# Kernel optimization log

Measured on AMD Instinct MI355X. Metric: run time of the kernel, lower is better.

## Reference

```python
import jax, jax.numpy as jnp
import numpy as np

DIM = 64
SQRT_DIM = float(np.sqrt(DIM))


def setup_inputs() -> dict:
    rng = jax.random.key(0)
    k1, k2, k3, k4 = jax.random.split(rng, 4)
    B, S, D = 16, 2048, DIM
    query = jax.random.normal(k1, (B, S, D), dtype=jnp.float32)
    key = jax.random.normal(k2, (B, S, D), dtype=jnp.float32)
    value = jax.random.normal(k3, (B, S, D), dtype=jnp.float32)
    mask = jax.random.randint(k4, (B, S), 0, 2) == 1  # True = masked (pad)
    return {"query": query, "key": key, "value": value, "mask": mask}


def reference(query, key, value, mask):
    # score: [B, S, S]
    score = jnp.einsum('bsd,btd->bst', query, key) / SQRT_DIM
    # symmetric mask: position (i, j) masked if token i OR token j is padded
    m = jnp.logical_or(mask[:, :, None], mask[:, None, :])  # [B, S, S]
    score = jnp.where(m, -jnp.inf, score)
    attn = jax.nn.softmax(score, axis=-1)
    attn = jnp.where(m, 0.0, attn)
    context = jnp.einsum('bst,btd->bsd', attn, value)
    return (context, attn)
```

## Files before the change

### kernel.cpp

```cpp
#include <hip/hip_runtime.h>
#include <hip/hip_bf16.h>

#define NBATCH 16
#define SLEN   2048
#define DIM    64
#define TQ     64
#define NTHR   256
#define NW     4
#define PANEL  128
#define NPANEL (SLEN / PANEL)
#define PROWK  72
#define PROWV  136
#define PROWP  136

typedef __attribute__((ext_vector_type(8))) short bf16x8;
typedef __attribute__((ext_vector_type(4))) float f32x4;

__device__ inline short f2bf(float f) {
    union { __hip_bfloat16 h; short s; } u;
    u.h = __float2bfloat16(f);
    return u.s;
}
__device__ inline float bf2f(unsigned short s) {
    union { unsigned u; float f; } x;
    x.u = ((unsigned)s) << 16;
    return x.f;
}
__device__ inline bf16x8 pack8(float4 a, float4 b) {
    bf16x8 r;
    r[0] = f2bf(a.x); r[1] = f2bf(a.y); r[2] = f2bf(a.z); r[3] = f2bf(a.w);
    r[4] = f2bf(b.x); r[5] = f2bf(b.y); r[6] = f2bf(b.z); r[7] = f2bf(b.w);
    return r;
}

__global__ __launch_bounds__(NTHR, 3) void sdpa_kernel(
    const float* __restrict__ Q, const float* __restrict__ K,
    const float* __restrict__ V, const int* __restrict__ M,
    float* __restrict__ outCtx, float* __restrict__ outAttn)
{
    __shared__ __align__(16) short sK[128 * PROWK];
    __shared__ __align__(16) short sVT[64 * PROWV];
    __shared__ __align__(16) short sP[NW * 16 * PROWP];
    __shared__ float sMask[PANEL];

    const int tid = threadIdx.x;
    const int w = tid >> 6, l = tid & 63, g = l >> 4, c = l & 15;
    const int b  = blockIdx.x >> 5;
    const int i0 = (blockIdx.x & 31) * TQ;
    const int i0w = i0 + w * 16;

    const float* Kb = K + (size_t)b * SLEN * DIM;
    const float* Vb = V + (size_t)b * SLEN * DIM;
    const int*   Mb = M + b * SLEN;

    bf16x8 qa0, qa1;
    {
        const float* qp = Q + ((size_t)b * SLEN + i0w + c) * DIM + g * 8;
        qa0 = pack8(*(const float4*)(qp),      *(const float4*)(qp + 4));
        qa1 = pack8(*(const float4*)(qp + 32), *(const float4*)(qp + 36));
    }

    const float scl = 0.125f;
    float rsum[4] = {0.f, 0.f, 0.f, 0.f};

    for (int p = 0; p < NPANEL; p++) {
        const int j0 = p * PANEL;
        #pragma unroll
        for (int it = 0; it < 8; it++) {
            const int idx = it * NTHR + tid;
            const int row = idx >> 4, c4 = idx & 15;
            float4 kv = *(const float4*)(Kb + (size_t)(j0 + row) * DIM + c4 * 4);
            *(short4*)(sK + row * PROWK + c4 * 4) =
                make_short4(f2bf(kv.x), f2bf(kv.y), f2bf(kv.z), f2bf(kv.w));
        }
        if (tid < PANEL) sMask[tid] = Mb[j0 + tid] ? 0.f : 1.f;
        __syncthreads();
        #pragma unroll
        for (int jt = 0; jt < 8; jt++) {
            const short* kr = sK + (jt * 16 + c) * PROWK + g * 8;
            bf16x8 kb0 = *(const bf16x8*)(kr);
            bf16x8 kb1 = *(const bf16x8*)(kr + 32);
            f32x4 acc = {0.f, 0.f, 0.f, 0.f};
            acc = __builtin_amdgcn_mfma_f32_16x16x32_bf16(qa0, kb0, acc, 0, 0, 0);
            acc = __builtin_amdgcn_mfma_f32_16x16x32_bf16(qa1, kb1, acc, 0, 0, 0);
            const float em = sMask[jt * 16 + c];
            #pragma unroll
            for (int r = 0; r < 4; r++)
                rsum[r] += __expf(acc[r] * scl) * em;
        }
        __syncthreads();
    }
    #pragma unroll
    for (int off = 1; off < 16; off <<= 1) {
        #pragma unroll
        for (int r = 0; r < 4; r++)
            rsum[r] += __shfl_xor(rsum[r], off, 64);
    }
    float scv[4];
    #pragma unroll
    for (int r = 0; r < 4; r++) {
        const int rm = Mb[i0w + g * 4 + r];
        scv[r] = (rm || rsum[r] <= 0.f) ? 0.f : 1.f / rsum[r];
    }

    short* sPw = sP + w * 16 * PROWP;
    f32x4 pv[4];
    #pragma unroll
    for (int nt = 0; nt < 4; nt++) pv[nt] = (f32x4){0.f, 0.f, 0.f, 0.f};

    for (int p = 0; p < NPANEL; p++) {
        const int j0 = p * PANEL;
        #pragma unroll
        for (int it = 0; it < 8; it++) {
            const int idx = it * NTHR + tid;
            const int row = idx >> 4, c4 = idx & 15;
            float4 kv = *(const float4*)(Kb + (size_t)(j0 + row) * DIM + c4 * 4);
            *(short4*)(sK + row * PROWK + c4 * 4) =
                make_short4(f2bf(kv.x), f2bf(kv.y), f2bf(kv.z), f2bf(kv.w));
        }
        #pragma unroll
        for (int it = 0; it < 2; it++) {
            const int task = it * NTHR + tid;
            const int k4 = task >> 4, d4g = task & 15;
            const int kb = k4 * 4, d4 = d4g * 4;
            const int colb = kb ^ ((d4g & 3) << 3);
            const float* vp = Vb + (size_t)(j0 + kb) * DIM + d4;
            float4 r0 = *(const float4*)(vp);
            float4 r1 = *(const float4*)(vp + DIM);
            float4 r2 = *(const float4*)(vp + 2 * DIM);
            float4 r3 = *(const float4*)(vp + 3 * DIM);
            *(short4*)(sVT + (d4 + 0) * PROWV + colb) =
                make_short4(f2bf(r0.x), f2bf(r1.x), f2bf(r2.x), f2bf(r3.x));
            *(short4*)(sVT + (d4 + 1) * PROWV + colb) =
                make_short4(f2bf(r0.y), f2bf(r1.y), f2bf(r2.y), f2bf(r3.y));
            *(short4*)(sVT + (d4 + 2) * PROWV + colb) =
                make_short4(f2bf(r0.z), f2bf(r1.z), f2bf(r2.z), f2bf(r3.z));
            *(short4*)(sVT + (d4 + 3) * PROWV + colb) =
                make_short4(f2bf(r0.w), f2bf(r1.w), f2bf(r2.w), f2bf(r3.w));
        }
        if (tid < PANEL) sMask[tid] = Mb[j0 + tid] ? 0.f : 1.f;
        __syncthreads();

        #pragma unroll
        for (int jt = 0; jt < 8; jt++) {
            const short* kr = sK + (jt * 16 + c) * PROWK + g * 8;
            bf16x8 kb0 = *(const bf16x8*)(kr);
            bf16x8 kb1 = *(const bf16x8*)(kr + 32);
            f32x4 acc = {0.f, 0.f, 0.f, 0.f};
            acc = __builtin_amdgcn_mfma_f32_16x16x32_bf16(qa0, kb0, acc, 0, 0, 0);
            acc = __builtin_amdgcn_mfma_f32_16x16x32_bf16(qa1, kb1, acc, 0, 0, 0);
            const float em = sMask[jt * 16 + c];
            #pragma unroll
            for (int r = 0; r < 4; r++)
                sPw[(g * 4 + r) * PROWP + jt * 16 + c] =
                    f2bf(__expf(acc[r] * scl) * em * scv[r]);
        }

        #pragma unroll
        for (int ks = 0; ks < 4; ks++) {
            bf16x8 af = *(const bf16x8*)(sPw + c * PROWP + ks * 32 + g * 8);
            #pragma unroll
            for (int nt = 0; nt < 4; nt++) {
                const int d = nt * 16 + c;
                const int gp = g ^ ((d >> 2) & 3);
                bf16x8 bfrag = *(const bf16x8*)(sVT + d * PROWV + ks * 32 + gp * 8);
                pv[nt] = __builtin_amdgcn_mfma_f32_16x16x32_bf16(af, bfrag, pv[nt], 0, 0, 0);
            }
        }

        const size_t rowBase = (size_t)b * SLEN + i0w;
        #pragma unroll
        for (int it = 0; it < 8; it++) {
            const int idx = it * 64 + l;
            const int row = idx >> 5, col4 = idx & 31;
            const unsigned short* pp = (const unsigned short*)sPw + row * PROWP + col4 * 4;
            ushort4 p4 = *(const ushort4*)(pp);
            float4 o = {bf2f(p4.x), bf2f(p4.y), bf2f(p4.z), bf2f(p4.w)};
            *(float4*)(outAttn + (rowBase + row) * SLEN + j0 + col4 * 4) = o;
        }
        __syncthreads();
    }

    #pragma unroll
    for (int nt = 0; nt < 4; nt++) {
        #pragma unroll
        for (int r = 0; r < 4; r++)
            outCtx[((size_t)b * SLEN + i0w + g * 4 + r) * DIM + nt * 16 + c] = pv[nt][r];
    }
}

extern "C" void kernel_launch(void* const* d_in, const int* in_sizes, int n_in,
                              void* d_out, int out_size, void* d_ws, size_t ws_size,
                              hipStream_t stream) {
    const float* Q = (const float*)d_in[0];
    const float* K = (const float*)d_in[1];
    const float* V = (const float*)d_in[2];
    const int*   M = (const int*)d_in[3];
    float* outCtx  = (float*)d_out;
    float* outAttn = (float*)d_out + (size_t)NBATCH * SLEN * DIM;
    dim3 grid(NBATCH * (SLEN / TQ));
    sdpa_kernel<<<grid, NTHR, 0, stream>>>(Q, K, V, M, outCtx, outAttn);
}
```

Before: 375.5 us.

## Preconvert K/V to swizzled bf16 workspace and stage panels via direct-to-LDS loads

Adds a pre-pass kernel that converts K to bf16 and V to transposed bf16 in a workspace, both XOR-swizzled, so every attention block no longer re-reads fp32 K/V and converts it for each panel. The main kernel stages panels with global_load_lds, double-buffers K during the row-sum pass, caches the whole mask row in LDS, and folds the 1/sqrt(d) scale into Q. It costs an extra kernel launch and workspace traffic, and lowers the occupancy hint from 3 to 2. A fallback keeps the original kernel when no workspace is available.

```diff
diff --git a/kernel.cpp b/kernel.cpp
--- a/kernel.cpp
+++ b/kernel.cpp
@@ -9,9 +9,9 @@
 #define NW     4
 #define PANEL  128
 #define NPANEL (SLEN / PANEL)
+#define PROWP  136
 #define PROWK  72
 #define PROWV  136
-#define PROWP  136
 
 typedef __attribute__((ext_vector_type(8))) short bf16x8;
 typedef __attribute__((ext_vector_type(4))) float f32x4;
@@ -32,8 +32,208 @@
     r[4] = f2bf(b.x); r[5] = f2bf(b.y); r[6] = f2bf(b.z); r[7] = f2bf(b.w);
     return r;
 }
-
-__global__ __launch_bounds__(NTHR, 3) void sdpa_kernel(
+__device__ inline bf16x8 pack8s(float4 a, float4 b, float s) {
+    bf16x8 r;
+    r[0] = f2bf(a.x * s); r[1] = f2bf(a.y * s); r[2] = f2bf(a.z * s); r[3] = f2bf(a.w * s);
+    r[4] = f2bf(b.x * s); r[5] = f2bf(b.y * s); r[6] = f2bf(b.z * s); r[7] = f2bf(b.w * s);
+    return r;
+}
+
+__global__ __launch_bounds__(256) void preconvert_kernel(
+    const float* __restrict__ K, const float* __restrict__ V,
+    short* __restrict__ Kws, short* __restrict__ VTws)
+{
+    const int b  = blockIdx.x >> 4;
+    const int p  = blockIdx.x & 15;
+    const int j0 = p * PANEL;
+    const int tid = threadIdx.x;
+    const float* Kb = K + ((size_t)b * SLEN + j0) * DIM;
+    const float* Vb = V + ((size_t)b * SLEN + j0) * DIM;
+    short* Kwb  = Kws  + ((size_t)b * SLEN + j0) * DIM;
+    short* VTwb = VTws + (size_t)b * DIM * SLEN;
+
+    #pragma unroll
+    for (int it = 0; it < 8; it++) {
+        const int idx = it * 256 + tid;
+        const int row = idx >> 4, c4 = idx & 15;
+        float4 kv = *(const float4*)(Kb + (size_t)row * DIM + c4 * 4);
+        const int blk = (c4 >> 1) ^ (row & 7);
+        *(short4*)(Kwb + (size_t)row * DIM + blk * 8 + (c4 & 1) * 4) =
+            make_short4(f2bf(kv.x), f2bf(kv.y), f2bf(kv.z), f2bf(kv.w));
+    }
+    #pragma unroll
+    for (int it = 0; it < 2; it++) {
+        const int task = it * 256 + tid;
+        const int k4 = task >> 4, d4 = (task & 15) * 4;
+        const int kb = k4 * 4;
+        const float* vp = Vb + (size_t)kb * DIM + d4;
+        float4 r0 = *(const float4*)(vp);
+        float4 r1 = *(const float4*)(vp + DIM);
+        float4 r2 = *(const float4*)(vp + 2 * DIM);
+        float4 r3 = *(const float4*)(vp + 3 * DIM);
+        const int qn = kb >> 3, hw = kb & 7;
+        *(short4*)(VTwb + (size_t)(d4 + 0) * SLEN + j0 + ((qn ^ ((d4 + 0) & 7)) * 8) + hw) =
+            make_short4(f2bf(r0.x), f2bf(r1.x), f2bf(r2.x), f2bf(r3.x));
+        *(short4*)(VTwb + (size_t)(d4 + 1) * SLEN + j0 + ((qn ^ ((d4 + 1) & 7)) * 8) + hw) =
+            make_short4(f2bf(r0.y), f2bf(r1.y), f2bf(r2.y), f2bf(r3.y));
+        *(short4*)(VTwb + (size_t)(d4 + 2) * SLEN + j0 + ((qn ^ ((d4 + 2) & 7)) * 8) + hw) =
+            make_short4(f2bf(r0.z), f2bf(r1.z), f2bf(r2.z), f2bf(r3.z));
+        *(short4*)(VTwb + (size_t)(d4 + 3) * SLEN + j0 + ((qn ^ ((d4 + 3) & 7)) * 8) + hw) =
+            make_short4(f2bf(r0.w), f2bf(r1.w), f2bf(r2.w), f2bf(r3.w));
+    }
+}
+
+__device__ __forceinline__ void stage_k_panel(const short* __restrict__ Kwb, int j0,
+                                              short* sdst, int w, int l) {
+    const short* src = Kwb + (size_t)j0 * DIM + w * 512 + l * 8;
+    short* dst = sdst + w * 512;
+    #pragma unroll
+    for (int i = 0; i < 4; i++)
+        __builtin_amdgcn_global_load_lds((const unsigned int*)(src + i * 2048),
+                                         (unsigned int*)(dst + i * 2048), 16, 0, 0);
+}
+__device__ __forceinline__ void stage_v_panel(const short* __restrict__ VTwb, int j0,
+                                              short* sdst, int w, int l) {
+    #pragma unroll
+    for (int i = 0; i < 4; i++) {
+        const int d0 = (w * 4 + i) * 4;
+        __builtin_amdgcn_global_load_lds(
+            (const unsigned int*)(VTwb + (size_t)(d0 + (l >> 4)) * SLEN + j0 + (l & 15) * 8),
+            (unsigned int*)(sdst + d0 * PANEL), 16, 0, 0);
+    }
+}
+
+#define MFMA16(a, bb, cc) __builtin_amdgcn_mfma_f32_16x16x32_bf16((a), (bb), (cc), 0, 0, 0)
+
+__global__ __launch_bounds__(NTHR, 2) void sdpa_kernel(
+    const float* __restrict__ Q, const short* __restrict__ Kws,
+    const short* __restrict__ VTws, const int* __restrict__ M,
+    float* __restrict__ outCtx, float* __restrict__ outAttn)
+{
+    __shared__ __align__(16) short sK[PANEL * DIM];
+    __shared__ __align__(16) short sVT[DIM * PANEL];
+    __shared__ __align__(16) short sP[NW * 16 * PROWP];
+    __shared__ float sMaskAll[SLEN];
+
+    const int tid = threadIdx.x;
+    const int w = tid >> 6, l = tid & 63, g = l >> 4, c = l & 15;
+    const int b  = blockIdx.x >> 5;
+    const int i0 = (blockIdx.x & 31) * TQ;
+    const int i0w = i0 + w * 16;
+
+    const short* Kwb  = Kws  + (size_t)b * SLEN * DIM;
+    const short* VTwb = VTws + (size_t)b * DIM * SLEN;
+    const int*   Mb   = M + b * SLEN;
+
+    bf16x8 qa0, qa1;
+    {
+        const float* qp = Q + ((size_t)b * SLEN + i0w + c) * DIM + g * 8;
+        qa0 = pack8s(*(const float4*)(qp),      *(const float4*)(qp + 4),  0.125f);
+        qa1 = pack8s(*(const float4*)(qp + 32), *(const float4*)(qp + 36), 0.125f);
+    }
+
+    #pragma unroll
+    for (int i = 0; i < 8; i++)
+        sMaskAll[i * NTHR + tid] = Mb[i * NTHR + tid] ? 0.f : 1.f;
+    stage_k_panel(Kwb, 0, sK, w, l);
+    __syncthreads();
+
+    float rsum[4] = {0.f, 0.f, 0.f, 0.f};
+    for (int p = 0; p < NPANEL; p++) {
+        const short* cur = (p & 1) ? sVT : sK;
+        if (p < NPANEL - 1)
+            stage_k_panel(Kwb, (p + 1) * PANEL, (p & 1) ? sK : sVT, w, l);
+        const int j0 = p * PANEL;
+        #pragma unroll
+        for (int jt = 0; jt < 8; jt++) {
+            const short* kr = cur + (jt * 16 + c) * DIM;
+            bf16x8 kb0 = *(const bf16x8*)(kr + ((g ^ (c & 7)) * 8));
+            bf16x8 kb1 = *(const bf16x8*)(kr + (((g + 4) ^ (c & 7)) * 8));
+            f32x4 acc = {0.f, 0.f, 0.f, 0.f};
+            acc = MFMA16(qa0, kb0, acc);
+            acc = MFMA16(qa1, kb1, acc);
+            const float em = sMaskAll[j0 + jt * 16 + c];
+            #pragma unroll
+            for (int r = 0; r < 4; r++)
+                rsum[r] += __expf(acc[r]) * em;
+        }
+        __syncthreads();
+    }
+    #pragma unroll
+    for (int off = 1; off < 16; off <<= 1) {
+        #pragma unroll
+        for (int r = 0; r < 4; r++)
+            rsum[r] += __shfl_xor(rsum[r], off, 64);
+    }
+    float scv[4];
+    #pragma unroll
+    for (int r = 0; r < 4; r++) {
+        const float rm = sMaskAll[i0w + g * 4 + r];
+        scv[r] = (rm == 0.f || rsum[r] <= 0.f) ? 0.f : 1.f / rsum[r];
+    }
+
+    short* sPw = sP + w * 16 * PROWP;
+    f32x4 pv[4];
+    #pragma unroll
+    for (int nt = 0; nt < 4; nt++) pv[nt] = (f32x4){0.f, 0.f, 0.f, 0.f};
+
+    stage_k_panel(Kwb, 0, sK, w, l);
+    stage_v_panel(VTwb, 0, sVT, w, l);
+    __syncthreads();
+
+    for (int p = 0; p < NPANEL; p++) {
+        const int j0 = p * PANEL;
+        #pragma unroll
+        for (int jt = 0; jt < 8; jt++) {
+            const short* kr = sK + (jt * 16 + c) * DIM;
+            bf16x8 kb0 = *(const bf16x8*)(kr + ((g ^ (c & 7)) * 8));
+            bf16x8 kb1 = *(const bf16x8*)(kr + (((g + 4) ^ (c & 7)) * 8));
+            f32x4 acc = {0.f, 0.f, 0.f, 0.f};
+            acc = MFMA16(qa0, kb0, acc);
+            acc = MFMA16(qa1, kb1, acc);
+            const float em = sMaskAll[j0 + jt * 16 + c];
+            #pragma unroll
+            for (int r = 0; r < 4; r++)
+                sPw[(g * 4 + r) * PROWP + jt * 16 + c] =
+                    f2bf(__expf(acc[r]) * em * scv[r]);
+        }
+        #pragma unroll
+        for (int ks = 0; ks < 4; ks++) {
+            bf16x8 af = *(const bf16x8*)(sPw + c * PROWP + ks * 32 + g * 8);
+            #pragma unroll
+            for (int nt = 0; nt < 4; nt++) {
+                const int d = nt * 16 + c;
+                bf16x8 bfrag = *(const bf16x8*)(sVT + d * PANEL + (((ks * 4 + g) ^ (d & 7)) * 8));
+                pv[nt] = MFMA16(af, bfrag, pv[nt]);
+            }
+        }
+        __syncthreads();
+        if (p < NPANEL - 1) {
+            stage_k_panel(Kwb, j0 + PANEL, sK, w, l);
+            stage_v_panel(VTwb, j0 + PANEL, sVT, w, l);
+        }
+        const size_t rowBase = (size_t)b * SLEN + i0w;
+        #pragma unroll
+        for (int it = 0; it < 8; it++) {
+            const int idx = it * 64 + l;
+            const int row = idx >> 5, col4 = idx & 31;
+            const unsigned short* pp = (const unsigned short*)sPw + row * PROWP + col4 * 4;
+            ushort4 p4 = *(const ushort4*)(pp);
+            float4 o = {bf2f(p4.x), bf2f(p4.y), bf2f(p4.z), bf2f(p4.w)};
+            *(float4*)(outAttn + (rowBase + row) * SLEN + j0 + col4 * 4) = o;
+        }
+        __syncthreads();
+    }
+
+    #pragma unroll
+    for (int nt = 0; nt < 4; nt++) {
+        #pragma unroll
+        for (int r = 0; r < 4; r++)
+            outCtx[((size_t)b * SLEN + i0w + g * 4 + r) * DIM + nt * 16 + c] = pv[nt][r];
+    }
+}
+
+__global__ __launch_bounds__(NTHR, 3) void sdpa_kernel_fb(
     const float* __restrict__ Q, const float* __restrict__ K,
     const float* __restrict__ V, const int* __restrict__ M,
     float* __restrict__ outCtx, float* __restrict__ outAttn)
@@ -81,8 +281,8 @@
             bf16x8 kb0 = *(const bf16x8*)(kr);
             bf16x8 kb1 = *(const bf16x8*)(kr + 32);
             f32x4 acc = {0.f, 0.f, 0.f, 0.f};
-            acc = __builtin_amdgcn_mfma_f32_16x16x32_bf16(qa0, kb0, acc, 0, 0, 0);
-            acc = __builtin_amdgcn_mfma_f32_16x16x32_bf16(qa1, kb1, acc, 0, 0, 0);
+            acc = MFMA16(qa0, kb0, acc);
+            acc = MFMA16(qa1, kb1, acc);
             const float em = sMask[jt * 16 + c];
             #pragma unroll
             for (int r = 0; r < 4; r++)
@@ -147,15 +347,14 @@
             bf16x8 kb0 = *(const bf16x8*)(kr);
             bf16x8 kb1 = *(const bf16x8*)(kr + 32);
             f32x4 acc = {0.f, 0.f, 0.f, 0.f};
-            acc = __builtin_amdgcn_mfma_f32_16x16x32_bf16(qa0, kb0, acc, 0, 0, 0);
-            acc = __builtin_amdgcn_mfma_f32_16x16x32_bf16(qa1, kb1, acc, 0, 0, 0);
+            acc = MFMA16(qa0, kb0, acc);
+            acc = MFMA16(qa1, kb1, acc);
             const float em = sMask[jt * 16 + c];
             #pragma unroll
             for (int r = 0; r < 4; r++)
                 sPw[(g * 4 + r) * PROWP + jt * 16 + c] =
                     f2bf(__expf(acc[r] * scl) * em * scv[r]);
         }
-
         #pragma unroll
         for (int ks = 0; ks < 4; ks++) {
             bf16x8 af = *(const bf16x8*)(sPw + c * PROWP + ks * 32 + g * 8);
@@ -164,10 +363,9 @@
                 const int d = nt * 16 + c;
                 const int gp = g ^ ((d >> 2) & 3);
                 bf16x8 bfrag = *(const bf16x8*)(sVT + d * PROWV + ks * 32 + gp * 8);
-                pv[nt] = __builtin_amdgcn_mfma_f32_16x16x32_bf16(af, bfrag, pv[nt], 0, 0, 0);
+                pv[nt] = MFMA16(af, bfrag, pv[nt]);
             }
         }
-
         const size_t rowBase = (size_t)b * SLEN + i0w;
         #pragma unroll
         for (int it = 0; it < 8; it++) {
@@ -199,5 +397,15 @@
     float* outCtx  = (float*)d_out;
     float* outAttn = (float*)d_out + (size_t)NBATCH * SLEN * DIM;
     dim3 grid(NBATCH * (SLEN / TQ));
-    sdpa_kernel<<<grid, NTHR, 0, stream>>>(Q, K, V, M, outCtx, outAttn);
-}
+
+    const size_t nElem = (size_t)NBATCH * SLEN * DIM;
+    const size_t wsNeed = nElem * 2 * sizeof(short);
+    if (d_ws != nullptr && ws_size >= wsNeed) {
+        short* Kws  = (short*)d_ws;
+        short* VTws = Kws + nElem;
+        preconvert_kernel<<<dim3(NBATCH * NPANEL), 256, 0, stream>>>(K, V, Kws, VTws);
+        sdpa_kernel<<<grid, NTHR, 0, stream>>>(Q, Kws, VTws, M, outCtx, outAttn);
+    } else {
+        sdpa_kernel_fb<<<grid, NTHR, 0, stream>>>(Q, K, V, M, outCtx, outAttn);
+    }
+}
```

Result: faster. 313.6 us (-16.5%).
